# Kernel optimization log

Measured on AMD Instinct MI355X. Metric: run time of the kernel, lower is better.

Reference implementation:

```python
import jax, jax.numpy as jnp
import numpy as np

# dims: batch N, channels C, fine nodes V, coarse nodes VC, super nodes S, time L
N, C, V, VC, S, L, CO = 16, 32, 2048, 256, 64, 12, 32
N1, N2, N3, N4 = 0.8, 0.2, 0.2, 0.2  # residual fusion scales


def asym_adj(a):
    # D^-1 A row-normalization (sp.diags(d_inv) @ A), inf -> 0
    rowsum = jnp.sum(a, axis=1)
    d_inv = jnp.where(rowsum > 0, 1.0 / rowsum, 0.0)
    return a * d_inv[:, None]


def nconv(x, a):
    return jnp.einsum('ncvl,vw->ncwl', x, a)


def gcn(x, supports, W, b):
    h = jnp.concatenate([x, nconv(x, supports[0]), nconv(x, supports[1])], axis=1)
    return jnp.einsum('nkvl,ok->novl', h, W) + b[None, :, None, None]


def hgcn_forward(x, support, support_c, acs, afc, W, b):
    hf = gcn(x, support, W, b)                               # fine level  [N,CO,V,L]
    xc = jnp.einsum('vw,ncvl->ncwl', afc, x)                 # afc.T @ x   [N,C,VC,L]
    hc = gcn(xc, support_c, W, b)                            # coarse level [N,CO,VC,L]
    sxg = jnp.einsum('ws,ncwl->ncsl', acs, xc)               # acs.T @ afc.T @ x [N,C,S,L]
    # faithful reproduction of torch permute/reshape (mismatched flatten orders)
    hs_flat = jnp.transpose(sxg, (2, 1, 0, 3)).reshape(S, -1)  # [S, C*N*L]
    hst = jnp.transpose(sxg, (3, 0, 1, 2)).reshape(-1, S)      # [L*N*C, S]
    as_mat = jax.lax.stop_gradient(jax.nn.relu(hs_flat @ hst - 0.5))  # detached [S,S]
    sup_s = [jax.nn.softmax(asym_adj(as_mat), axis=-1),
             jax.nn.softmax(asym_adj(as_mat.T), axis=-1)]
    hs = gcn(sxg, sup_s, W, b)                               # super level [N,CO,S,L]
    # hierarchical relu-scaled residual fusions
    hc = hc + N1 * jax.nn.relu(jnp.einsum('ws,ncsl->ncwl', acs, hs))
    hf = hf + N2 * jax.nn.relu(jnp.einsum('vw,ncwl->ncvl', afc, hc))
    hc = hc + N3 * jax.nn.relu(jnp.einsum('vw,ncvl->ncwl', afc, hf))
    hs = hs + N4 * jax.nn.relu(jnp.einsum('ws,ncwl->ncsl', acs, hc))
    return hf, hc, hs


def setup_inputs() -> dict:
    key = jax.random.key(0)
    k = jax.random.split(key, 7)
    x = jax.random.normal(k[0], (N, C, V, L), jnp.float32)
    support = jax.nn.softmax(jax.random.normal(k[1], (2, V, V), jnp.float32), axis=-1)
    support_c = jax.nn.softmax(jax.random.normal(k[2], (2, VC, VC), jnp.float32), axis=-1)
    acs = jax.random.normal(k[3], (VC, S), jnp.float32) * 0.05
    afc = jax.random.normal(k[4], (V, VC), jnp.float32) * 0.02
    W = jax.random.normal(k[5], (CO, 3 * C), jnp.float32) * 0.05  # 1x1 conv weight
    b = jax.random.normal(k[6], (CO,), jnp.float32) * 0.01
    return {"x": x, "support": support, "support_c": support_c, "acs": acs,
            "afc": afc, "W": W, "b": b}


def reference(x, support, support_c, acs, afc, W, b):
    return hgcn_forward(x, support, support_c, acs, afc, W, b)
```

## Files before the change

kernel.cpp:

```cpp
#include <hip/hip_runtime.h>

constexpr int NB = 16;
constexpr int CC = 32;
constexpr int VV = 2048;
constexpr int VCC = 256;
constexpr int SS = 64;
constexpr int LL = 12;
constexpr int CO = 32;
constexpr long MM = (long)NB * CO * LL;

typedef __attribute__((ext_vector_type(8))) __bf16 bf16x8;
typedef __attribute__((ext_vector_type(4))) float f32x4;

__device__ __forceinline__ unsigned short f2bf(float f) {
    unsigned u = __float_as_uint(f);
    unsigned r = u + 0x7FFFu + ((u >> 16) & 1u);
    return (unsigned short)(r >> 16);
}

__device__ __forceinline__ void gl_lds16(const void* g, void* l) {
    __builtin_amdgcn_global_load_lds(
        (const __attribute__((address_space(1))) void*)g,
        (__attribute__((address_space(3))) void*)l, 16, 0, 0);
}

__global__ __launch_bounds__(256)
void transpose_vl(const float* __restrict__ in, float* __restrict__ out,
                  unsigned short* __restrict__ outb) {
    __shared__ float t[128 * 12];
    const long nc = blockIdx.y;
    const int v0 = blockIdx.x * 128;
    const float* src = in + (nc * VV + v0) * 12;
    for (int f = threadIdx.x; f < 128 * 12; f += 256) t[f] = src[f];
    __syncthreads();
    float* dst = out + nc * 12L * VV;
    unsigned short* dstb = outb + nc * 12L * VV;
    for (int g = threadIdx.x; g < 128 * 12; g += 256) {
        int l = g >> 7, vv = g & 127;
        const float v = t[vv * 12 + l];
        dst[(long)l * VV + v0 + vv] = v;
        dstb[(long)l * VV + v0 + vv] = f2bf(v);
    }
}

__global__ __launch_bounds__(256)
void transpose_lv(const float* __restrict__ in, float* __restrict__ out, int Kn, int TW) {
    __shared__ float t[128 * 12];
    const long nc = blockIdx.y;
    const int v0 = blockIdx.x * TW;
    const float* src = in + nc * 12L * Kn;
    for (int g = threadIdx.x; g < TW * 12; g += 256) {
        int l = g / TW, vv = g - l * TW;
        t[vv * 12 + l] = src[(long)l * Kn + v0 + vv];
    }
    __syncthreads();
    float* dst = out + (nc * Kn + v0) * 12L;
    for (int f = threadIdx.x; f < TW * 12; f += 256) dst[f] = t[f];
}

__global__ __launch_bounds__(256)
void transpose2d(const float* __restrict__ in, float* __restrict__ out, int rows, int cols) {
    __shared__ float t[32][33];
    const int r0 = blockIdx.y * 32, c0 = blockIdx.x * 32;
    const int ty = threadIdx.x / 32, tx = threadIdx.x % 32;
    for (int i = ty; i < 32; i += 8) t[i][tx] = in[(long)(r0 + i) * cols + c0 + tx];
    __syncthreads();
    for (int i = ty; i < 32; i += 8) out[(long)(c0 + i) * rows + r0 + tx] = t[tx][i];
}

__global__ __launch_bounds__(256)
void cvt_T_bf16_k(const float* __restrict__ in, unsigned short* __restrict__ out,
                  int R, int Ccols) {
    __shared__ float t[32][33];
    const int r0 = blockIdx.y * 32, c0 = blockIdx.x * 32;
    const int ty = threadIdx.x / 32, tx = threadIdx.x % 32;
    for (int i = ty; i < 32; i += 8) t[i][tx] = in[(long)(r0 + i) * Ccols + c0 + tx];
    __syncthreads();
    for (int i = ty; i < 32; i += 8) out[(long)(c0 + i) * R + r0 + tx] = f2bf(t[tx][i]);
}

__global__ __launch_bounds__(256)
void cvt_afc_both(const float* __restrict__ in, unsigned short* __restrict__ outn,
                  unsigned short* __restrict__ outt) {
    __shared__ float t[32][33];
    const int r0 = blockIdx.y * 32, c0 = blockIdx.x * 32;
    const int ty = threadIdx.x / 32, tx = threadIdx.x % 32;
    for (int i = ty; i < 32; i += 8) {
        const float v = in[(long)(r0 + i) * VCC + c0 + tx];
        t[i][tx] = v;
        outn[(long)(r0 + i) * VCC + c0 + tx] = f2bf(v);
    }
    __syncthreads();
    for (int i = ty; i < 32; i += 8) out_store:
        outt[(long)(c0 + i) * VV + r0 + tx] = f2bf(t[tx][i]);
}

__global__ __launch_bounds__(256)
void chanmix_fine(const float* __restrict__ in, const float* __restrict__ Wt,
                  float* __restrict__ y0, unsigned short* __restrict__ y12) {
    __shared__ float Ws[CO * 96];
    for (int idx = threadIdx.x; idx < CO * 96; idx += 256) Ws[idx] = Wt[idx];
    __syncthreads();
    const int nb = blockIdx.y;
    const int r = blockIdx.x * 256 + threadIdx.x;
    const int R = LL * VV;
    const int l = r / VV, k = r - l * VV;
    float xv[CC];
#pragma unroll
    for (int c = 0; c < CC; ++c) xv[c] = in[((long)(nb * CC + c)) * R + r];
    for (int o = 0; o < CO; ++o) {
        float a0 = 0.f, a1 = 0.f, a2 = 0.f;
#pragma unroll
        for (int c = 0; c < CC; ++c) {
            const float x = xv[c];
            a0 = fmaf(Ws[o * 96 + c], x, a0);
            a1 = fmaf(Ws[o * 96 + 32 + c], x, a1);
            a2 = fmaf(Ws[o * 96 + 64 + c], x, a2);
        }
        const long mrow = (long)(nb * CO + o) * LL + l;
        y0[mrow * VV + k] = a0;
        y12[mrow * 4096 + k] = f2bf(a1);
        y12[mrow * 4096 + 2048 + k] = f2bf(a2);
    }
}

__global__ __launch_bounds__(256)
void chanmix_k(const float* __restrict__ in, const float* __restrict__ Wt,
               int R, int Kn, float* __restrict__ o0,
               float* __restrict__ o1, int ld1) {
    __shared__ float Ws[CO * 96];
    for (int idx = threadIdx.x; idx < CO * 96; idx += 256) Ws[idx] = Wt[idx];
    __syncthreads();
    const int nb = blockIdx.y;
    const int r = blockIdx.x * 256 + threadIdx.x;
    if (r >= R) return;
    const int l = r / Kn, k = r - l * Kn;
    float xv[CC];
#pragma unroll
    for (int c = 0; c < CC; ++c) xv[c] = in[((long)(nb * CC + c)) * R + r];
    for (int o = 0; o < CO; ++o) {
        float a0 = 0.f, a1 = 0.f, a2 = 0.f;
#pragma unroll
        for (int c = 0; c < CC; ++c) {
            const float x = xv[c];
            a0 = fmaf(Ws[o * 96 + c], x, a0);
            a1 = fmaf(Ws[o * 96 + 32 + c], x, a1);
            a2 = fmaf(Ws[o * 96 + 64 + c], x, a2);
        }
        const long mrow = (long)(nb * CO + o) * LL + l;
        o0[mrow * Kn + k] = a0;
        o1[mrow * ld1 + k] = a1;
        o1[mrow * ld1 + Kn + k] = a2;
    }
}

template <int BN, bool SWIZ, bool RELU, bool ADDC0, bool BIAS, bool STB16>
__global__ __launch_bounds__(256)
void gemm_mfma(const unsigned short* __restrict__ A, int lda,
               const unsigned short* __restrict__ Bt, int ldb,
               const float* __restrict__ C0, int ldc,
               const float* __restrict__ bias,
               float* __restrict__ Out, int ldo,
               unsigned short* __restrict__ OutB, int K, float alpha) {
    constexpr int TNT = BN / 32;
    constexpr int QB = BN / 32;
    constexpr int WN = BN / 2;
    __shared__ __align__(16) unsigned short As[128 * 64];
    __shared__ __align__(16) unsigned short Bs[BN * 64];
    const int tid = threadIdx.x;
    const int lane = tid & 63;
    const int w = tid >> 6;

    int pid_m, pid_n;
    if constexpr (SWIZ) {
        const int id = blockIdx.y * gridDim.x + blockIdx.x;
        const int npg = 8 * gridDim.x;
        const int rem = id % npg;
        pid_m = (id / npg) * 8 + (rem & 7);
        pid_n = rem >> 3;
    } else {
        pid_m = blockIdx.y;
        pid_n = blockIdx.x;
    }
    const long m0 = (long)pid_m * 128;
    const int n0 = pid_n * BN;

    long offA[4], offB[QB];
#pragma unroll
    for (int q = 0; q < 4; ++q) {
        const int t = q * 256 + tid;
        const int row = t >> 3, pos = t & 7;
        const int lc = pos ^ (row & 7);
        offA[q] = (m0 + row) * (long)lda + lc * 8;
    }
#pragma unroll
    for (int q = 0; q < QB; ++q) {
        const int t = q * 256 + tid;
        const int row = t >> 3, pos = t & 7;
        const int lc = pos ^ (row & 7);
        offB[q] = (long)(n0 + row) * ldb + lc * 8;
    }
    const int wm = (w & 1) * 64, wn = (w >> 1) * WN;
    const int mrow = lane & 15;
    const int quad = lane >> 4;

    f32x4 acc[4][TNT];
#pragma unroll
    for (int i = 0; i < 4; ++i)
#pragma unroll
        for (int j = 0; j < TNT; ++j) acc[i][j] = (f32x4){0.f, 0.f, 0.f, 0.f};

    for (int k0 = 0; k0 < K; k0 += 64) {
#pragma unroll
        for (int q = 0; q < 4; ++q)
            gl_lds16(A + offA[q] + k0, &As[(q * 256 + w * 64) * 8]);
#pragma unroll
        for (int q = 0; q < QB; ++q)
            gl_lds16(Bt + offB[q] + k0, &Bs[(q * 256 + w * 64) * 8]);
        __syncthreads();
#pragma unroll
        for (int ks = 0; ks < 2; ++ks) {
            bf16x8 af[4], bfr[TNT];
            const int pos = (ks * 4 + quad) ^ (mrow & 7);
#pragma unroll
            for (int tm = 0; tm < 4; ++tm) {
                const int r = wm + tm * 16 + mrow;
                af[tm] = *(const bf16x8*)&As[r * 64 + pos * 8];
            }
#pragma unroll
            for (int tn = 0; tn < TNT; ++tn) {
                const int r = wn + tn * 16 + mrow;
                bfr[tn] = *(const bf16x8*)&Bs[r * 64 + pos * 8];
            }
#pragma unroll
            for (int tm = 0; tm < 4; ++tm)
#pragma unroll
                for (int tn = 0; tn < TNT; ++tn)
                    acc[tm][tn] = __builtin_amdgcn_mfma_f32_16x16x32_bf16(
                        af[tm], bfr[tn], acc[tm][tn], 0, 0, 0);
        }
        __syncthreads();
    }

#pragma unroll
    for (int tm = 0; tm < 4; ++tm) {
#pragma unroll
        for (int tn = 0; tn < TNT; ++tn) {
            const int n = n0 + wn + tn * 16 + mrow;
#pragma unroll
            for (int reg = 0; reg < 4; ++reg) {
                const long m = m0 + wm + tm * 16 + quad * 4 + reg;
                float p = acc[tm][tn][reg];
                if (RELU) p = fmaxf(p, 0.f);
                p *= alpha;
                float c = 0.f;
                if constexpr (ADDC0) c = C0[m * (long)ldc + n];
                if (BIAS) c += bias[(int)((m / LL) & (CO - 1))];
                const float res = c + p;
                Out[m * (long)ldo + n] = res;
                if constexpr (STB16) OutB[m * (long)ldo + n] = f2bf(res);
            }
        }
    }
}

template <int BM, int BN, int BK, int TM, int TN, bool RELU, bool ADDC0, bool BIAS, bool STB16>
__global__ __launch_bounds__(256)
void gemm_k(const float* __restrict__ X, int ldx,
            const float* __restrict__ Bm, int ldb,
            const float* __restrict__ C0, int ldc,
            const float* __restrict__ bias,
            float* __restrict__ Out, int ldo,
            unsigned short* __restrict__ outb, int K, float alpha) {
    constexpr int TX = BN / TN;
    constexpr int LX = (BM * BK) / 256;
    constexpr int LB = (BN * BK) / 256;
    __shared__ float Xs[BK][BM + 4];
    __shared__ float Bs[BK][BN + 4];
    const int tid = threadIdx.x;
    const int tx = tid % TX, ty = tid / TX;
    const long m0 = (long)blockIdx.y * BM;
    const int n0 = blockIdx.x * BN;
    const int xr = tid / (BK / LX);
    const int xcc = (tid % (BK / LX)) * LX;
    const int br = tid / (BN / LB);
    const int bc = (tid % (BN / LB)) * LB;

    float acc[TM][TN];
#pragma unroll
    for (int i = 0; i < TM; ++i)
#pragma unroll
        for (int j = 0; j < TN; ++j) acc[i][j] = 0.f;

    const float* Xp = X + (m0 + xr) * (long)ldx + xcc;
    const float* Bp = Bm + (long)br * ldb + n0 + bc;

    for (int k0 = 0; k0 < K; k0 += BK) {
        if constexpr (LX == 4) {
            const float4 v = *(const float4*)Xp;
            Xs[xcc + 0][xr] = v.x; Xs[xcc + 1][xr] = v.y;
            Xs[xcc + 2][xr] = v.z; Xs[xcc + 3][xr] = v.w;
        } else {
            const float2 v = *(const float2*)Xp;
            Xs[xcc + 0][xr] = v.x; Xs[xcc + 1][xr] = v.y;
        }
        if constexpr (LB == 4) {
            *(float4*)&Bs[br][bc] = *(const float4*)Bp;
        } else {
            *(float2*)&Bs[br][bc] = *(const float2*)Bp;
        }
        __syncthreads();
#pragma unroll
        for (int kk = 0; kk < BK; ++kk) {
            float a[TM], b[TN];
#pragma unroll
            for (int i = 0; i < TM; ++i) a[i] = Xs[kk][ty * TM + i];
#pragma unroll
            for (int j = 0; j < TN; ++j) b[j] = Bs[kk][tx * TN + j];
#pragma unroll
            for (int i = 0; i < TM; ++i)
#pragma unroll
                for (int j = 0; j < TN; ++j) acc[i][j] = fmaf(a[i], b[j], acc[i][j]);
        }
        __syncthreads();
        Xp += BK;
        Bp += (long)BK * ldb;
    }

#pragma unroll
    for (int i = 0; i < TM; ++i) {
        const long m = m0 + (long)ty * TM + i;
        float bv = 0.f;
        if (BIAS) bv = bias[(int)((m / LL) & (CO - 1))];
        const long obase = m * (long)ldo + n0 + tx * TN;
        long cbase = 0;
        if constexpr (ADDC0) cbase = m * (long)ldc + n0 + tx * TN;
#pragma unroll
        for (int j = 0; j < TN; ++j) {
            float p = acc[i][j];
            if (RELU) p = fmaxf(p, 0.f);
            p *= alpha;
            float c = 0.f;
            if constexpr (ADDC0) c = C0[cbase + j];
            const float res = c + p + bv;
            Out[obase + j] = res;
            if constexpr (STB16) outb[obase + j] = f2bf(res);
        }
    }
}

__global__ __launch_bounds__(256)
void zero_k(float* __restrict__ p, int n) {
    for (int i = blockIdx.x * 256 + threadIdx.x; i < n; i += gridDim.x * 256) p[i] = 0.f;
}

__global__ __launch_bounds__(256)
void asmat_split(const float* __restrict__ sxg, float* __restrict__ am_raw) {
    __shared__ float Us[128][65];
    __shared__ float Wsh[128][65];
    __shared__ int rA[128], rB[128];
    const int i0 = blockIdx.x * 128;
    const int tid = threadIdx.x;
    if (tid < 128) {
        const int i = i0 + tid;
        const int c = i / 192;
        const int rem = i - c * 192;
        const int n = rem / 12;
        const int l = rem - n * 12;
        rA[tid] = (n * 32 + c) * 12 + l;
        const int l2 = i >> 9;
        const int rem2 = i & 511;
        rB[tid] = ((rem2 >> 5) * 32 + (rem2 & 31)) * 12 + l2;
    }
    __syncthreads();
    for (int idx = tid; idx < 128 * 64; idx += 256) {
        const int r = idx >> 6, s = idx & 63;
        Us[r][s] = sxg[rA[r] * 64 + s];
        Wsh[r][s] = sxg[rB[r] * 64 + s];
    }
    __syncthreads();
    const int ts = (tid & 15) * 4;
    const int tt = (tid >> 4) * 4;
    float acc[4][4];
#pragma unroll
    for (int i2 = 0; i2 < 4; ++i2)
#pragma unroll
        for (int j = 0; j < 4; ++j) acc[i2][j] = 0.f;
    for (int k = 0; k < 128; ++k) {
        float a[4], bv[4];
#pragma unroll
        for (int i2 = 0; i2 < 4; ++i2) a[i2] = Us[k][ts + i2];
#pragma unroll
        for (int j = 0; j < 4; ++j) bv[j] = Wsh[k][tt + j];
#pragma unroll
        for (int i2 = 0; i2 < 4; ++i2)
#pragma unroll
            for (int j = 0; j < 4; ++j) acc[i2][j] = fmaf(a[i2], bv[j], acc[i2][j]);
    }
#pragma unroll
    for (int i2 = 0; i2 < 4; ++i2)
#pragma unroll
        for (int j = 0; j < 4; ++j)
            atomicAdd(&am_raw[(ts + i2) * 64 + tt + j], acc[i2][j]);
}

__global__ __launch_bounds__(64)
void supbuild_k(const float* __restrict__ am_raw, float* __restrict__ sup) {
    __shared__ float a[64][65];
    for (int idx = threadIdx.x; idx < 4096; idx += 64) {
        const float v = am_raw[idx] - 0.5f;
        a[idx >> 6][idx & 63] = v > 0.f ? v : 0.f;
    }
    __syncthreads();
    const int r = threadIdx.x;
    {
        float rs = 0.f;
        for (int j = 0; j < 64; ++j) rs += a[r][j];
        const float dinv = rs > 0.f ? 1.f / rs : 0.f;
        float mx = -1e30f;
        for (int j = 0; j < 64; ++j) mx = fmaxf(mx, a[r][j] * dinv);
        float se = 0.f;
        for (int j = 0; j < 64; ++j) se += expf(a[r][j] * dinv - mx);
        const float inv = 1.f / se;
        for (int j = 0; j < 64; ++j) sup[r * 64 + j] = expf(a[r][j] * dinv - mx) * inv;
    }
    {
        float rs = 0.f;
        for (int j = 0; j < 64; ++j) rs += a[j][r];
        const float dinv = rs > 0.f ? 1.f / rs : 0.f;
        float mx = -1e30f;
        for (int j = 0; j < 64; ++j) mx = fmaxf(mx, a[j][r] * dinv);
        float se = 0.f;
        for (int j = 0; j < 64; ++j) se += expf(a[j][r] * dinv - mx);
        const float inv = 1.f / se;
        for (int j = 0; j < 64; ++j) sup[4096 + r * 64 + j] = expf(a[j][r] * dinv - mx) * inv;
    }
}

extern "C" void kernel_launch(void* const* d_in, const int* in_sizes, int n_in,
                              void* d_out, int out_size, void* d_ws, size_t ws_size,
                              hipStream_t stream) {
    (void)in_sizes; (void)n_in; (void)out_size; (void)ws_size;
    const float* x    = (const float*)d_in[0];
    const float* sup  = (const float*)d_in[1];
    const float* supc = (const float*)d_in[2];
    const float* acs  = (const float*)d_in[3];
    const float* afc  = (const float*)d_in[4];
    const float* W    = (const float*)d_in[5];
    const float* b    = (const float*)d_in[6];
    float* ws = (float*)d_ws;

    float* xt = ws;
    unsigned short* Btu = (unsigned short*)ws;
    float* yc0  = ws + 4456448;
    float* yc12 = ws + 6029312;
    float* ys0  = ws + 9175040;
    float* ys12 = ws + 9568256;
    float* hc   = ws + 10354688;
    float* hs   = ws + 11927552;
    float* am   = ws + 12320768;
    float* sups = ws + 12324864;
    float* acsT = ws + 12333056;
    float* hf   = ws + 12582912;
    float* xc   = ws + 25165824;
    float* sxg  = ws + 26738688;
    unsigned short* afcTb = (unsigned short*)(ws + 27131904);
    unsigned short* afcb  = (unsigned short*)(ws + 27394048);

    float* out_f = (float*)d_out;
    unsigned short* xtb  = (unsigned short*)d_out;
    unsigned short* y12u = (unsigned short*)d_out;
    unsigned short* hfb  = (unsigned short*)d_out;
    unsigned short* hcb  = ((unsigned short*)d_out) + 12582912;
    float* hf_out = out_f;
    float* hc_out = out_f + 12582912;
    float* hs_out = out_f + 14155776;

    transpose_vl<<<dim3(VV / 128, NB * CC), 256, 0, stream>>>(x, xt, xtb);
    cvt_afc_both<<<dim3(VCC / 32, VV / 32), 256, 0, stream>>>(afc, afcb, afcTb);
    gemm_mfma<64, false, false, false, false, false><<<dim3(VCC / 64, MM / 128), 256, 0, stream>>>(
        xtb, VV, afcTb, VV, nullptr, 0, nullptr, xc, VCC, nullptr, VV, 1.0f);
    chanmix_fine<<<dim3(96, 16), 256, 0, stream>>>(xt, W, hf, y12u);
    cvt_T_bf16_k<<<dim3(VV / 32, 2 * VV / 32), 256, 0, stream>>>(sup, Btu, 2 * VV, VV);
    gemm_k<64, 64, 16, 4, 4, false, false, false, false><<<dim3(1, MM / 64), 256, 0, stream>>>(
        xc, VCC, acs, SS, nullptr, 0, nullptr, sxg, SS, nullptr, VCC, 1.0f);
    chanmix_k<<<dim3(12, 16), 256, 0, stream>>>(xc, W, LL * VCC, VCC, yc0, yc12, 2 * VCC);
    chanmix_k<<<dim3(3, 16), 256, 0, stream>>>(sxg, W, LL * SS, SS, ys0, ys12, 2 * SS);
    zero_k<<<dim3(4), 256, 0, stream>>>(am, 4096);
    asmat_split<<<dim3(48), 256, 0, stream>>>(sxg, am);
    supbuild_k<<<dim3(1), 64, 0, stream>>>(am, sups);
    gemm_mfma<128, true, false, true, true, false><<<dim3(VV / 128, MM / 128), 256, 0, stream>>>(
        y12u, 4096, Btu, 4096, hf, VV, b, hf, VV, nullptr, 4096, 1.0f);
    gemm_k<64, 64, 16, 4, 4, false, true, true, false><<<dim3(VCC / 64, MM / 64), 256, 0, stream>>>(
        yc12, 2 * VCC, supc, VCC, yc0, VCC, b, hc, VCC, nullptr, 2 * VCC, 1.0f);
    gemm_k<64, 64, 16, 4, 4, false, true, true, false><<<dim3(1, MM / 64), 256, 0, stream>>>(
        ys12, 2 * SS, sups, SS, ys0, SS, b, hs, SS, nullptr, 2 * SS, 1.0f);
    transpose2d<<<dim3(SS / 32, VCC / 32), 256, 0, stream>>>(acs, acsT, VCC, SS);
    gemm_k<64, 64, 16, 4, 4, true, true, false, true><<<dim3(VCC / 64, MM / 64), 256, 0, stream>>>(
        hs, SS, acsT, VCC, hc, VCC, nullptr, hc, VCC, hcb, SS, 0.8f);
    gemm_mfma<128, true, true, true, false, true><<<dim3(VV / 128, MM / 128), 256, 0, stream>>>(
        hcb, VCC, afcb, VCC, hf, VV, nullptr, hf, VV, hfb, VCC, 0.2f);
    gemm_mfma<64, false, true, true, false, false><<<dim3(VCC / 64, MM / 128), 256, 0, stream>>>(
        hfb, VV, afcTb, VV, hc, VCC, nullptr, hc, VCC, nullptr, VV, 0.2f);
    gemm_k<64, 64, 16, 4, 4, true, true, false, false><<<dim3(1, MM / 64), 256, 0, stream>>>(
        hc, VCC, acs, SS, hs, SS, nullptr, hs, SS, nullptr, VCC, 0.2f);
    transpose_lv<<<dim3(VV / 128, NB * CO), 256, 0, stream>>>(hf, hf_out, VV, 128);
    transpose_lv<<<dim3(VCC / 128, NB * CO), 256, 0, stream>>>(hc, hc_out, VCC, 128);
    transpose_lv<<<dim3(1, NB * CO), 256, 0, stream>>>(hs, hs_out, SS, 64);
}
```

Baseline: 647.8 us.

## Add 256x256-tile double-buffered bf16 MFMA GEMM for fine-level support product

```diff
diff --git a/kernel.cpp b/kernel.cpp
--- a/kernel.cpp
+++ b/kernel.cpp
@@ -91,7 +91,7 @@
         outn[(long)(r0 + i) * VCC + c0 + tx] = f2bf(v);
     }
     __syncthreads();
-    for (int i = ty; i < 32; i += 8) out_store:
+    for (int i = ty; i < 32; i += 8)
         outt[(long)(c0 + i) * VV + r0 + tx] = f2bf(t[tx][i]);
 }
 
@@ -259,6 +259,146 @@
                 const float res = c + p;
                 Out[m * (long)ldo + n] = res;
                 if constexpr (STB16) OutB[m * (long)ldo + n] = f2bf(res);
+            }
+        }
+    }
+}
+
+__global__ __launch_bounds__(512)
+void gemm_mfma256(const unsigned short* __restrict__ A, int lda,
+                  const unsigned short* __restrict__ Bt, int ldb,
+                  const float* __restrict__ C0, int ldc,
+                  const float* __restrict__ bias,
+                  float* __restrict__ Out, int ldo, int K) {
+    __shared__ __align__(16) unsigned short As[2][256 * 64];
+    __shared__ __align__(16) unsigned short Bs[2][256 * 64];
+    const int tid = threadIdx.x;
+    const int lane = tid & 63;
+    const int w = tid >> 6;
+    const int wr = w >> 2;
+    const int wc = w & 3;
+    const int mrow = lane & 15;
+    const int quad = lane >> 4;
+
+    const long m0 = (long)blockIdx.y * 256;
+    const int n0 = blockIdx.x * 256;
+
+    long offA[2][2], offB[2][2];
+#pragma unroll
+    for (int h = 0; h < 2; ++h)
+#pragma unroll
+        for (int q = 0; q < 2; ++q) {
+            const int t = q * 512 + tid;
+            const int row = t >> 3, pos = t & 7;
+            const int lc = pos ^ (row & 7);
+            offA[h][q] = (m0 + h * 128 + row) * (long)lda + lc * 8;
+            offB[h][q] = (long)(n0 + h * 128 + row) * ldb + lc * 8;
+        }
+    const int NT = K >> 6;
+
+#define STAGE_A(b_, t_, h_)                                                  \
+    do {                                                                     \
+        gl_lds16(A + offA[h_][0] + (long)(t_) * 64,                          \
+                 &As[b_][(h_) * 8192 + w * 512]);                            \
+        gl_lds16(A + offA[h_][1] + (long)(t_) * 64,                          \
+                 &As[b_][(h_) * 8192 + 4096 + w * 512]);                     \
+    } while (0)
+#define STAGE_B(b_, t_, h_)                                                  \
+    do {                                                                     \
+        gl_lds16(Bt + offB[h_][0] + (long)(t_) * 64,                         \
+                 &Bs[b_][(h_) * 8192 + w * 512]);                            \
+        gl_lds16(Bt + offB[h_][1] + (long)(t_) * 64,                         \
+                 &Bs[b_][(h_) * 8192 + 4096 + w * 512]);                     \
+    } while (0)
+
+    const int p0 = (quad ^ (mrow & 7)) * 8;
+    const int p1 = ((4 + quad) ^ (mrow & 7)) * 8;
+    const int ra = (wr * 128 + mrow) * 64;
+    const int rb = (wc * 64 + mrow) * 64;
+
+    f32x4 acc[8][4];
+#pragma unroll
+    for (int i = 0; i < 8; ++i)
+#pragma unroll
+        for (int j = 0; j < 4; ++j) acc[i][j] = (f32x4){0.f, 0.f, 0.f, 0.f};
+
+    STAGE_A(0, 0, 0); STAGE_A(0, 0, 1);
+    STAGE_B(0, 0, 0); STAGE_B(0, 0, 1);
+    if (NT > 1) {
+        STAGE_A(1, 1, 0); STAGE_A(1, 1, 1);
+        STAGE_B(1, 1, 0);
+        asm volatile("s_waitcnt vmcnt(6)" ::: "memory");
+    } else {
+        asm volatile("s_waitcnt vmcnt(0)" ::: "memory");
+    }
+    __builtin_amdgcn_sched_barrier(0);
+    __builtin_amdgcn_s_barrier();
+    __builtin_amdgcn_sched_barrier(0);
+
+    for (int t = 0; t < NT; ++t) {
+        const int buf = t & 1;
+        bf16x8 a0[8], b0[4], a1[8], b1[4];
+#pragma unroll
+        for (int tm = 0; tm < 8; ++tm)
+            a0[tm] = *(const bf16x8*)&As[buf][ra + tm * 1024 + p0];
+#pragma unroll
+        for (int tn = 0; tn < 4; ++tn)
+            b0[tn] = *(const bf16x8*)&Bs[buf][rb + tn * 1024 + p0];
+        if (t + 1 < NT) { STAGE_B(buf ^ 1, t + 1, 1); }
+        __builtin_amdgcn_s_setprio(1);
+#pragma unroll
+        for (int tm = 0; tm < 8; ++tm)
+#pragma unroll
+            for (int tn = 0; tn < 4; ++tn)
+                acc[tm][tn] = __builtin_amdgcn_mfma_f32_16x16x32_bf16(
+                    a0[tm], b0[tn], acc[tm][tn], 0, 0, 0);
+        __builtin_amdgcn_s_setprio(0);
+#pragma unroll
+        for (int tm = 0; tm < 8; ++tm)
+            a1[tm] = *(const bf16x8*)&As[buf][ra + tm * 1024 + p1];
+#pragma unroll
+        for (int tn = 0; tn < 4; ++tn)
+            b1[tn] = *(const bf16x8*)&Bs[buf][rb + tn * 1024 + p1];
+        asm volatile("s_waitcnt lgkmcnt(0)" ::: "memory");
+        __builtin_amdgcn_sched_barrier(0);
+        __builtin_amdgcn_s_barrier();
+        __builtin_amdgcn_sched_barrier(0);
+        if (t + 2 < NT) {
+            STAGE_A(buf, t + 2, 0); STAGE_A(buf, t + 2, 1);
+            STAGE_B(buf, t + 2, 0);
+        }
+        __builtin_amdgcn_s_setprio(1);
+#pragma unroll
+        for (int tm = 0; tm < 8; ++tm)
+#pragma unroll
+            for (int tn = 0; tn < 4; ++tn)
+                acc[tm][tn] = __builtin_amdgcn_mfma_f32_16x16x32_bf16(
+                    a1[tm], b1[tn], acc[tm][tn], 0, 0, 0);
+        __builtin_amdgcn_s_setprio(0);
+        if (t + 2 < NT) {
+            asm volatile("s_waitcnt vmcnt(6)" ::: "memory");
+        } else if (t + 1 < NT) {
+            asm volatile("s_waitcnt vmcnt(0)" ::: "memory");
+        }
+        __builtin_amdgcn_sched_barrier(0);
+        __builtin_amdgcn_s_barrier();
+        __builtin_amdgcn_sched_barrier(0);
+    }
+#undef STAGE_A
+#undef STAGE_B
+
+#pragma unroll
+    for (int tm = 0; tm < 8; ++tm) {
+#pragma unroll
+        for (int tn = 0; tn < 4; ++tn) {
+            const int n = n0 + wc * 64 + tn * 16 + mrow;
+#pragma unroll
+            for (int reg = 0; reg < 4; ++reg) {
+                const long m = m0 + wr * 128 + tm * 16 + quad * 4 + reg;
+                float p = acc[tm][tn][reg];
+                float c = C0[m * (long)ldc + n];
+                c += bias[(int)((m / LL) & (CO - 1))];
+                Out[m * (long)ldo + n] = c + p;
             }
         }
     }
@@ -489,8 +629,8 @@
     zero_k<<<dim3(4), 256, 0, stream>>>(am, 4096);
     asmat_split<<<dim3(48), 256, 0, stream>>>(sxg, am);
     supbuild_k<<<dim3(1), 64, 0, stream>>>(am, sups);
-    gemm_mfma<128, true, false, true, true, false><<<dim3(VV / 128, MM / 128), 256, 0, stream>>>(
-        y12u, 4096, Btu, 4096, hf, VV, b, hf, VV, nullptr, 4096, 1.0f);
+    gemm_mfma256<<<dim3(VV / 256, MM / 256), 512, 0, stream>>>(
+        y12u, 4096, Btu, 4096, hf, VV, b, hf, VV, 4096);
     gemm_k<64, 64, 16, 4, 4, false, true, true, false><<<dim3(VCC / 64, MM / 64), 256, 0, stream>>>(
         yc12, 2 * VCC, supc, VCC, yc0, VCC, b, hc, VCC, nullptr, 2 * VCC, 1.0f);
     gemm_k<64, 64, 16, 4, 4, false, true, true, false><<<dim3(1, MM / 64), 256, 0, stream>>>(
```

Measured after the change: 648.8 us. About the same (+0.1%).
